# Performance work log

Measured on AMD Instinct MI355X. Metric: run time of the kernel, lower is better.

The kernel has to match this reference:

```python
import jax, jax.numpy as jnp
import numpy as np

N = 100000
E = 1600000
D = 128

NEG_SLOPE = 0.1


def _leaky(x):
    return jnp.where(x >= 0, x, NEG_SLOPE * x)


def _ising_gcn(x, row, col, val, n, W=None, b=None, bias=None):
    # scatter_mean of |val| over source rows -> custom diagonal
    abs_val = jnp.abs(val)
    cnt = jax.ops.segment_sum(jnp.ones_like(abs_val), row, num_segments=n)
    abs_mean = jax.ops.segment_sum(abs_val, row, num_segments=n) / jnp.maximum(cnt, 1.0)
    diag = jnp.arange(n, dtype=row.dtype)
    frow = jnp.concatenate([row, diag])
    fcol = jnp.concatenate([col, diag])
    fval = jnp.concatenate([val, abs_mean])
    # symmetric normalization on |values|: v / sqrt(deg[row] * deg[col])
    deg = jax.ops.segment_sum(jnp.abs(fval), frow, num_segments=n)
    dinv = jnp.where(deg > 0, jax.lax.rsqrt(deg), 0.0)
    pv = fval * dinv[frow] * dinv[fcol]
    if W is not None:
        x = x @ W.T + b
    # propagate: out[col] += pv * x[row]  (PyG source_to_target, aggr='add')
    out = jax.ops.segment_sum(pv[:, None] * x[frow], fcol, num_segments=n)
    if bias is not None:
        out = out + bias
    return out


def setup_inputs() -> dict:
    key = jax.random.key(0)
    ks = jax.random.split(key, 10)
    edge_index = jax.random.randint(ks[0], (2, E), 0, N, dtype=jnp.int64)
    edge_val = jax.random.normal(ks[1], (E,), dtype=jnp.float32)
    s1 = 1.0 / np.sqrt(1.0)
    s2 = 1.0 / np.sqrt(D)
    s3 = 1.0 / np.sqrt(2 * D)
    return {
        "edge_index": edge_index,
        "edge_val": edge_val,
        "n_nodes": N,
        "w1": jax.random.uniform(ks[2], (D, 1), jnp.float32, -s1, s1),
        "b1": jax.random.uniform(ks[3], (D,), jnp.float32, -s1, s1),
        "w2": jax.random.uniform(ks[4], (2 * D, D), jnp.float32, -s2, s2),
        "b2": jax.random.uniform(ks[5], (2 * D,), jnp.float32, -s2, s2),
        "bias2": jnp.zeros((2 * D,), jnp.float32),
        "w3": jax.random.uniform(ks[6], (D, 2 * D), jnp.float32, -s3, s3),
        "b3": jax.random.uniform(ks[7], (D,), jnp.float32, -s3, s3),
        "bias3": jnp.zeros((D,), jnp.float32),
    }


def reference(edge_index, edge_val, n_nodes, w1, b1, w2, b2, bias2, w3, b3, bias3):
    row, col = edge_index[0], edge_index[1]
    x = jnp.ones((n_nodes, 1), dtype=edge_val.dtype)
    # conv1: no W, no bias (1 -> 1)
    x = _ising_gcn(x, row, col, edge_val, n_nodes)
    # linear 1 -> D, leaky relu (dropout omitted: inference)
    x = _leaky(x @ w1.T + b1)
    # conv2: D -> 2D with lin + bias
    x = _leaky(_ising_gcn(x, row, col, edge_val, n_nodes, W=w2, b=b2, bias=bias2))
    # conv3: 2D -> D with lin + bias
    x = _leaky(_ising_gcn(x, row, col, edge_val, n_nodes, W=w3, b=b3, bias=bias3))
    return x
```

## Files before the change

### kernel.cpp

```cpp
#include <hip/hip_runtime.h>
#include <hip/hip_bf16.h>

#define NEG_SLOPE 0.1f
#define D1 128
#define D2 256

#define BSH 7
#define NPB 128
#define EPB 2048
#define MAXBUK 1024

__device__ __forceinline__ float leaky(float x) { return x >= 0.f ? x : NEG_SLOPE * x; }

__device__ __forceinline__ unsigned short f2bf(float x) {
    union { float f; unsigned int u; } v; v.f = x;
    unsigned int r = (v.u + 0x7FFFu + ((v.u >> 16) & 1u)) >> 16;
    return (unsigned short)r;
}

__device__ __forceinline__ unsigned int pk2bf(float a, float b) {
    return (unsigned int)f2bf(a) | ((unsigned int)f2bf(b) << 16);
}

__device__ __forceinline__ int ts_g(const int* __restrict__ TS,
                                    const int* __restrict__ partials, int idx) {
    return TS[idx] + partials[idx >> 11];
}

__global__ __launch_bounds__(256) void k_hist(const int* __restrict__ row,
                                              const int* __restrict__ col,
                                              int* __restrict__ T,
                                              int E, int NBLK, int NBUK)
{
    __shared__ int hc[MAXBUK], hr[MAXBUK];
    for (int b = threadIdx.x; b < NBUK; b += 256) { hc[b] = 0; hr[b] = 0; }
    __syncthreads();
    int base = blockIdx.x * EPB;
#pragma unroll
    for (int i = 0; i < 8; i++) {
        int e = base + i * 256 + threadIdx.x;
        if (e < E) {
            atomicAdd(&hc[col[e] >> BSH], 1);
            atomicAdd(&hr[row[e] >> BSH], 1);
        }
    }
    __syncthreads();
    int NT = NBUK * NBLK;
    for (int b = threadIdx.x; b < NBUK; b += 256) {
        T[b * NBLK + blockIdx.x]      = hc[b];
        T[NT + b * NBLK + blockIdx.x] = hr[b];
    }
}

__global__ __launch_bounds__(256) void k_scan_local(const int* __restrict__ in, int* __restrict__ out,
                                                    int* __restrict__ partials, int n)
{
    __shared__ int s[256];
    int base = blockIdx.x * 2048 + threadIdx.x * 8;
    int v[8]; int sum = 0;
#pragma unroll
    for (int i = 0; i < 8; i++) { v[i] = (base + i < n) ? in[base + i] : 0; sum += v[i]; }
    s[threadIdx.x] = sum;
    __syncthreads();
    for (int off = 1; off < 256; off <<= 1) {
        int t = (threadIdx.x >= off) ? s[threadIdx.x - off] : 0;
        __syncthreads();
        s[threadIdx.x] += t;
        __syncthreads();
    }
    int excl = s[threadIdx.x] - sum;
#pragma unroll
    for (int i = 0; i < 8; i++) { if (base + i < n) { out[base + i] = excl; excl += v[i]; } }
    if (threadIdx.x == 255) partials[blockIdx.x] = s[255];
}

__global__ __launch_bounds__(1024) void k_scan_partials_par(int* __restrict__ partials, int nb)
{
    __shared__ int s[1024];
    int t = threadIdx.x;
    int v = (t < nb) ? partials[t] : 0;
    s[t] = v;
    __syncthreads();
    for (int off = 1; off < 1024; off <<= 1) {
        int u = (t >= off) ? s[t - off] : 0;
        __syncthreads();
        s[t] += u;
        __syncthreads();
    }
    if (t < nb) partials[t] = s[t] - v;
}

__global__ __launch_bounds__(256) void k_scat(const int* __restrict__ row,
                                              const int* __restrict__ col,
                                              const float* __restrict__ val,
                                              const int* __restrict__ TS,
                                              const int* __restrict__ partials,
                                              int2* __restrict__ X, int2* __restrict__ Y,
                                              int E, int NBLK, int NBUK)
{
    __shared__ int oc[MAXBUK], orw[MAXBUK];
    int NT = NBUK * NBLK;
    for (int b = threadIdx.x; b < NBUK; b += 256) {
        oc[b]  = ts_g(TS, partials, b * NBLK + blockIdx.x);
        orw[b] = ts_g(TS, partials, NT + b * NBLK + blockIdx.x);
    }
    __syncthreads();
    int base = blockIdx.x * EPB;
#pragma unroll
    for (int i = 0; i < 8; i++) {
        int e = base + i * 256 + threadIdx.x;
        if (e < E) {
            int r = row[e], c = col[e];
            float v = val[e];
            int pc = atomicAdd(&oc[c >> BSH], 1);
            X[pc] = make_int2(((c & (NPB - 1)) << 25) | r, __float_as_int(v));
            int pr = atomicAdd(&orw[r >> BSH], 1);
            Y[pr - E] = make_int2(r & (NPB - 1), __float_as_int(fabsf(v)));
        }
    }
}

__global__ __launch_bounds__(256) void k_rowstats(const int2* __restrict__ Y,
                                                  const int* __restrict__ TS,
                                                  const int* __restrict__ partials,
                                                  float* __restrict__ dinv,
                                                  float* __restrict__ pv_self,
                                                  int N, int E, int NBLK, int NBUK)
{
    __shared__ float fs[NPB];
    __shared__ int   cn[NPB];
    int t = threadIdx.x;
    if (t < NPB) { fs[t] = 0.f; cn[t] = 0; }
    __syncthreads();
    int NT = NBUK * NBLK;
    int buk = blockIdx.x;
    int s = ts_g(TS, partials, NT + buk * NBLK);
    int e = (buk == NBUK - 1) ? 2 * E : ts_g(TS, partials, NT + (buk + 1) * NBLK);
    for (int j = s + t; j < e; j += 256) {
        int2 y = Y[j - E];
        atomicAdd(&fs[y.x], __int_as_float(y.y));
        atomicAdd(&cn[y.x], 1);
    }
    __syncthreads();
    if (t < NPB) {
        int node = buk * NPB + t;
        if (node < N) {
            float as = fs[t];
            float c  = (float)cn[t];
            float am = as / fmaxf(c, 1.f);
            float deg = as + am;
            float di = deg > 0.f ? rsqrtf(deg) : 0.f;
            dinv[node]    = di;
            pv_self[node] = am * di * di;
        }
    }
}

__global__ __launch_bounds__(256) void k_colfinal(const int2* __restrict__ X,
                                                  const int* __restrict__ TS,
                                                  const int* __restrict__ partials,
                                                  const float* __restrict__ dinv,
                                                  const float* __restrict__ pv_self,
                                                  int* __restrict__ col_ptr,
                                                  int2* __restrict__ srt_rp,
                                                  float* __restrict__ x1,
                                                  int N, int E, int NBLK, int NBUK)
{
    __shared__ int   hist[NPB];
    __shared__ int   tmp[NPB];
    __shared__ int   rb[NPB];
    __shared__ float xs[NPB];
    __shared__ float dl[NPB];
    int t = threadIdx.x;
    int buk = blockIdx.x;
    int node = buk * NPB + t;
    if (t < NPB) {
        hist[t] = 0; xs[t] = 0.f;
        dl[t] = (node < N) ? dinv[node] : 0.f;
    }
    __syncthreads();
    int s  = ts_g(TS, partials, buk * NBLK);
    int e2 = (buk == NBUK - 1) ? E : ts_g(TS, partials, (buk + 1) * NBLK);
    for (int j = s + t; j < e2; j += 256) {
        unsigned xw = (unsigned)X[j].x;
        atomicAdd(&hist[xw >> 25], 1);
    }
    __syncthreads();
    if (t < NPB) tmp[t] = hist[t];
    __syncthreads();
    for (int off = 1; off < NPB; off <<= 1) {
        int u = (t >= off && t < NPB) ? tmp[t - off] : 0;
        __syncthreads();
        if (t < NPB) tmp[t] += u;
        __syncthreads();
    }
    if (t < NPB) {
        int excl = tmp[t] - hist[t];
        rb[t] = s + excl;
        if (node < N) col_ptr[node] = s + excl;
    }
    if (buk == NBUK - 1 && t == 0) col_ptr[N] = E;
    __syncthreads();
    for (int j = s + t; j < e2; j += 256) {
        int2 xx = X[j];
        unsigned xw = (unsigned)xx.x;
        int cl = xw >> 25;
        int r  = (int)(xw & 0x1FFFFFFu);
        float p = __int_as_float(xx.y) * dinv[r] * dl[cl];
        int pos = atomicAdd(&rb[cl], 1);
        srt_rp[pos] = make_int2(r, __float_as_int(p));
        atomicAdd(&xs[cl], p);
    }
    __syncthreads();
    if (t < NPB && node < N) x1[node] = pv_self[node] + xs[t];
}

__global__ __launch_bounds__(256) void k_prop2b(const int* __restrict__ col_ptr,
                                                const int2* __restrict__ srt_rp,
                                                const float* __restrict__ pv_self,
                                                const float* __restrict__ x1,
                                                const float* __restrict__ w1,
                                                const float* __restrict__ b1,
                                                unsigned int* __restrict__ p2b, int N)
{
    int node = blockIdx.x * 4 + (threadIdx.x >> 6);
    int lane = threadIdx.x & 63;
    if (node >= N) return;

    float2 w = *(const float2*)&w1[lane * 2];
    float2 b = *(const float2*)&b1[lane * 2];
    float ps  = pv_self[node];
    float x1n = x1[node];
    float acc0 = ps * leaky(fmaf(x1n, w.x, b.x));
    float acc1 = ps * leaky(fmaf(x1n, w.y, b.y));

    int s = col_ptr[node], e = col_ptr[node + 1];
    for (int base = s; base < e; base += 64) {
        int mc = min(64, e - base);
        float p = 0.f, sv = 0.f;
        if (lane < mc) {
            int2 rp = srt_rp[base + lane];
            p  = __int_as_float(rp.y);
            sv = x1[rp.x];
        }
        for (int k = 0; k < mc; ++k) {
            float pk = __shfl(p, k, 64);
            float sk = __shfl(sv, k, 64);
            acc0 += pk * leaky(fmaf(sk, w.x, b.x));
            acc1 += pk * leaky(fmaf(sk, w.y, b.y));
        }
    }

    p2b[(size_t)node * 64 + lane] = pk2bf(acc0, acc1);
}

__global__ __launch_bounds__(256) void k_prop3_bf16(const int* __restrict__ col_ptr,
                                                    const int2* __restrict__ srt_rp,
                                                    const float* __restrict__ pv_self,
                                                    const unsigned int* __restrict__ zb,
                                                    const float* __restrict__ bias3,
                                                    float* __restrict__ out, int N)
{
    int node = blockIdx.x * 4 + (threadIdx.x >> 6);
    int lane = threadIdx.x & 63;
    if (node >= N) return;

    unsigned int us = zb[(size_t)node * 64 + lane];
    float ps = pv_self[node];
    float acc0 = ps * __uint_as_float(us << 16);
    float acc1 = ps * __uint_as_float(us & 0xFFFF0000u);

    int j = col_ptr[node], e = col_ptr[node + 1];
    for (; j + 3 < e; j += 4) {
        int2 rp0 = srt_rp[j];
        int2 rp1 = srt_rp[j + 1];
        int2 rp2 = srt_rp[j + 2];
        int2 rp3 = srt_rp[j + 3];
        unsigned int u0 = zb[(size_t)rp0.x * 64 + lane];
        unsigned int u1 = zb[(size_t)rp1.x * 64 + lane];
        unsigned int u2 = zb[(size_t)rp2.x * 64 + lane];
        unsigned int u3 = zb[(size_t)rp3.x * 64 + lane];
        float p0 = __int_as_float(rp0.y);
        float p1 = __int_as_float(rp1.y);
        float p2 = __int_as_float(rp2.y);
        float p3 = __int_as_float(rp3.y);
        acc0 += p0 * __uint_as_float(u0 << 16);
        acc1 += p0 * __uint_as_float(u0 & 0xFFFF0000u);
        acc0 += p1 * __uint_as_float(u1 << 16);
        acc1 += p1 * __uint_as_float(u1 & 0xFFFF0000u);
        acc0 += p2 * __uint_as_float(u2 << 16);
        acc1 += p2 * __uint_as_float(u2 & 0xFFFF0000u);
        acc0 += p3 * __uint_as_float(u3 << 16);
        acc1 += p3 * __uint_as_float(u3 & 0xFFFF0000u);
    }
    for (; j < e; ++j) {
        int2 rp = srt_rp[j];
        unsigned int u = zb[(size_t)rp.x * 64 + lane];
        float p = __int_as_float(rp.y);
        acc0 += p * __uint_as_float(u << 16);
        acc1 += p * __uint_as_float(u & 0xFFFF0000u);
    }

    float2 b = *(const float2*)&bias3[lane * 2];
    float2 o = make_float2(leaky(acc0 + b.x), leaky(acc1 + b.y));
    *(float2*)&out[(size_t)node * D1 + lane * 2] = o;
}

__global__ __launch_bounds__(256) void k_gemm_fused(const unsigned int* __restrict__ p2b,
                                                    const float* __restrict__ w2,
                                                    const float* __restrict__ b2,
                                                    const float* __restrict__ bias2,
                                                    const float* __restrict__ w3,
                                                    const float* __restrict__ b3,
                                                    const float* __restrict__ x1,
                                                    unsigned short* __restrict__ zb,
                                                    int N)
{
    typedef __attribute__((ext_vector_type(8))) short short8v;
    typedef __attribute__((ext_vector_type(4))) float f32x4;

    __shared__ unsigned short Al[64 * 40];
    __shared__ unsigned short Bl[256 * 40];
    __shared__ unsigned short H[64 * 264];

    const int t = threadIdx.x;
    const int n_base = blockIdx.x * 64;
    const int l  = t & 63, wid = t >> 6;
    const int lr = l & 15,  lk = l >> 4;

    f32x4 acc1[4][4] = {};
    {
        const int arow = t >> 2, ach = t & 3;
        const bool aok = (n_base + arow) < N;
        for (int k0 = 0; k0 < D1; k0 += 32) {
            uint4 ua = make_uint4(0u, 0u, 0u, 0u);
            if (aok) ua = *(const uint4*)&p2b[(size_t)(n_base + arow) * 64 + (k0 >> 1) + ach * 4];
            const float* pw = w2 + (size_t)t * D1 + k0;
            float4 c0 = *(const float4*)(pw);
            float4 c1 = *(const float4*)(pw + 4);
            float4 c2 = *(const float4*)(pw + 8);
            float4 c3 = *(const float4*)(pw + 12);
            float4 c4 = *(const float4*)(pw + 16);
            float4 c5 = *(const float4*)(pw + 20);
            float4 c6 = *(const float4*)(pw + 24);
            float4 c7 = *(const float4*)(pw + 28);
            __syncthreads();
            *(uint4*)&Al[arow * 40 + ach * 8] = ua;
            uint4 u0 = make_uint4(pk2bf(c0.x, c0.y), pk2bf(c0.z, c0.w),
                                  pk2bf(c1.x, c1.y), pk2bf(c1.z, c1.w));
            uint4 u1 = make_uint4(pk2bf(c2.x, c2.y), pk2bf(c2.z, c2.w),
                                  pk2bf(c3.x, c3.y), pk2bf(c3.z, c3.w));
            uint4 u2 = make_uint4(pk2bf(c4.x, c4.y), pk2bf(c4.z, c4.w),
                                  pk2bf(c5.x, c5.y), pk2bf(c5.z, c5.w));
            uint4 u3 = make_uint4(pk2bf(c6.x, c6.y), pk2bf(c6.z, c6.w),
                                  pk2bf(c7.x, c7.y), pk2bf(c7.z, c7.w));
            *(uint4*)&Bl[t * 40 + 0]  = u0;
            *(uint4*)&Bl[t * 40 + 8]  = u1;
            *(uint4*)&Bl[t * 40 + 16] = u2;
            *(uint4*)&Bl[t * 40 + 24] = u3;
            __syncthreads();

            short8v af[4], bf[4];
#pragma unroll
            for (int i = 0; i < 4; i++) {
                af[i] = *(const short8v*)&Al[(i * 16 + lr) * 40 + lk * 8];
                bf[i] = *(const short8v*)&Bl[(wid * 64 + i * 16 + lr) * 40 + lk * 8];
            }
#pragma unroll
            for (int i = 0; i < 4; i++)
#pragma unroll
                for (int j = 0; j < 4; j++)
                    acc1[i][j] = __builtin_amdgcn_mfma_f32_16x16x32_bf16(af[i], bf[j], acc1[i][j], 0, 0, 0);
        }
    }

    {
        float xv[4][4];
#pragma unroll
        for (int i = 0; i < 4; i++)
#pragma unroll
            for (int q = 0; q < 4; q++) {
                int node = n_base + i * 16 + lk * 4 + q;
                xv[i][q] = (node < N) ? x1[node] : 0.f;
            }
#pragma unroll
        for (int j = 0; j < 4; j++) {
            const int col = wid * 64 + j * 16 + lr;
            const float bv = b2[col];
            const float bi = bias2[col];
#pragma unroll
            for (int i = 0; i < 4; i++)
#pragma unroll
                for (int q = 0; q < 4; q++) {
                    int rloc = i * 16 + lk * 4 + q;
                    float v = acc1[i][j][q] + xv[i][q] * bv + bi;
                    H[rloc * 264 + col] = ((n_base + rloc) < N) ? f2bf(leaky(v)) : (unsigned short)0;
                }
        }
    }
    __syncthreads();

    f32x4 acc2[4][2] = {};
    {
        const int m = t >> 1, hf = t & 1;
        for (int k0 = 0; k0 < D2; k0 += 32) {
            const float* pw = w3 + (size_t)m * D2 + k0 + hf * 16;
            float4 c0 = *(const float4*)(pw);
            float4 c1 = *(const float4*)(pw + 4);
            float4 c2 = *(const float4*)(pw + 8);
            float4 c3 = *(const float4*)(pw + 12);
            __syncthreads();
            uint4 u0 = make_uint4(pk2bf(c0.x, c0.y), pk2bf(c0.z, c0.w),
                                  pk2bf(c1.x, c1.y), pk2bf(c1.z, c1.w));
            uint4 u1 = make_uint4(pk2bf(c2.x, c2.y), pk2bf(c2.z, c2.w),
                                  pk2bf(c3.x, c3.y), pk2bf(c3.z, c3.w));
            *(uint4*)&Bl[m * 40 + hf * 16 + 0] = u0;
            *(uint4*)&Bl[m * 40 + hf * 16 + 8] = u1;
            __syncthreads();

            short8v af[4], bf[2];
#pragma unroll
            for (int i = 0; i < 4; i++)
                af[i] = *(const short8v*)&H[(i * 16 + lr) * 264 + k0 + lk * 8];
#pragma unroll
            for (int j = 0; j < 2; j++)
                bf[j] = *(const short8v*)&Bl[(wid * 32 + j * 16 + lr) * 40 + lk * 8];
#pragma unroll
            for (int i = 0; i < 4; i++)
#pragma unroll
                for (int j = 0; j < 2; j++)
                    acc2[i][j] = __builtin_amdgcn_mfma_f32_16x16x32_bf16(af[i], bf[j], acc2[i][j], 0, 0, 0);
        }
    }

#pragma unroll
    for (int j = 0; j < 2; j++) {
        const int col = wid * 32 + j * 16 + lr;
        const float bv = b3[col];
#pragma unroll
        for (int i = 0; i < 4; i++)
#pragma unroll
            for (int q = 0; q < 4; q++) {
                int node = n_base + i * 16 + lk * 4 + q;
                if (node < N)
                    zb[(size_t)node * D1 + col] = f2bf(acc2[i][j][q] + bv);
            }
    }
}

extern "C" void kernel_launch(void* const* d_in, const int* in_sizes, int n_in,
                              void* d_out, int out_size, void* d_ws, size_t ws_size,
                              hipStream_t stream)
{
    const int* ei       = (const int*)d_in[0];
    const float* val    = (const float*)d_in[1];
    const float* w1     = (const float*)d_in[3];
    const float* b1     = (const float*)d_in[4];
    const float* w2     = (const float*)d_in[5];
    const float* b2     = (const float*)d_in[6];
    const float* bias2  = (const float*)d_in[7];
    const float* w3     = (const float*)d_in[8];
    const float* b3     = (const float*)d_in[9];
    const float* bias3  = (const float*)d_in[10];
    float* out = (float*)d_out;

    const int E = in_sizes[1];
    const int N = out_size / D1;
    const int* row = ei;
    const int* col = ei + E;

    const int NBLK = (E + EPB - 1) / EPB;
    const int NBUK = (N + NPB - 1) >> BSH;
    const int NT   = NBUK * NBLK;

    float* dinv    = (float*)d_ws;
    float* pv_self = dinv + N;
    float* x1      = pv_self + N;
    int*   col_ptr = (int*)(x1 + N);
    int*   partials= col_ptr + N + 8;
    int2*  srt_rp  = (int2*)(partials + 1024);
    unsigned int* p2b = (unsigned int*)(srt_rp + (size_t)E);
    int*   TS      = (int*)(p2b + (size_t)N * 64);
    int*   T       = TS + (size_t)2 * NT;
    int2*  Y       = (int2*)(T + (size_t)2 * NT);
    int2* X = (int2*)p2b;
    unsigned short* zb = (unsigned short*)p2b;

    const int B = 256;
    const int n2 = 2 * NT;
    const int scan_blocks = (n2 + 2047) / 2048;

    k_hist<<<NBLK, B, 0, stream>>>(row, col, T, E, NBLK, NBUK);
    k_scan_local<<<scan_blocks, 256, 0, stream>>>(T, TS, partials, n2);
    k_scan_partials_par<<<1, 1024, 0, stream>>>(partials, scan_blocks);
    k_scat<<<NBLK, B, 0, stream>>>(row, col, val, TS, partials, X, Y, E, NBLK, NBUK);
    k_rowstats<<<NBUK, B, 0, stream>>>(Y, TS, partials, dinv, pv_self, N, E, NBLK, NBUK);
    k_colfinal<<<NBUK, B, 0, stream>>>(X, TS, partials, dinv, pv_self, col_ptr, srt_rp, x1, N, E, NBLK, NBUK);

    k_prop2b<<<(N + 3) / 4, 256, 0, stream>>>(col_ptr, srt_rp, pv_self, x1, w1, b1, p2b, N);
    k_gemm_fused<<<(N + 63) / 64, 256, 0, stream>>>(p2b, w2, b2, bias2, w3, b3, x1, zb, N);

    k_prop3_bf16<<<(N + 3) / 4, 256, 0, stream>>>(col_ptr, srt_rp, pv_self, (const unsigned int*)zb, bias3, out, N);
}
```

Measured before the change: 413.7 us.

## Pre-convert weights to MFMA-ready bf16 layout and drop per-block weight staging

```diff
diff --git a/kernel.cpp b/kernel.cpp
--- a/kernel.cpp
+++ b/kernel.cpp
@@ -306,145 +306,132 @@
     *(float2*)&out[(size_t)node * D1 + lane * 2] = o;
 }
 
-__global__ __launch_bounds__(256) void k_gemm_fused(const unsigned int* __restrict__ p2b,
-                                                    const float* __restrict__ w2,
-                                                    const float* __restrict__ b2,
-                                                    const float* __restrict__ bias2,
-                                                    const float* __restrict__ w3,
-                                                    const float* __restrict__ b3,
-                                                    const float* __restrict__ x1,
-                                                    unsigned short* __restrict__ zb,
-                                                    int N)
+__global__ __launch_bounds__(256) void k_cvtw(const float* __restrict__ w2,
+                                              const float* __restrict__ w3,
+                                              unsigned short* __restrict__ w2f,
+                                              unsigned short* __restrict__ w3f)
+{
+    int i = blockIdx.x * 256 + threadIdx.x;
+    {
+        int m = i >> 7, k = i & 127;
+        w2f[(((k >> 3) * 256 + m) << 3) + (k & 7)] = f2bf(w2[i]);
+    }
+    {
+        int m = i >> 8, k = i & 255;
+        w3f[(((k >> 3) * 128 + m) << 3) + (k & 7)] = f2bf(w3[i]);
+    }
+}
+
+__global__ __launch_bounds__(256, 3) void k_gemm_fused2(const unsigned int* __restrict__ p2b,
+                                                        const unsigned short* __restrict__ w2f,
+                                                        const float* __restrict__ b2,
+                                                        const float* __restrict__ bias2,
+                                                        const unsigned short* __restrict__ w3f,
+                                                        const float* __restrict__ b3,
+                                                        const float* __restrict__ x1,
+                                                        unsigned short* __restrict__ zb,
+                                                        int N)
 {
     typedef __attribute__((ext_vector_type(8))) short short8v;
     typedef __attribute__((ext_vector_type(4))) float f32x4;
 
-    __shared__ unsigned short Al[64 * 40];
-    __shared__ unsigned short Bl[256 * 40];
-    __shared__ unsigned short H[64 * 264];
+    __shared__ unsigned short Ak[16 * 64 * 8];
+    __shared__ unsigned short H [32 * 64 * 8];
 
     const int t = threadIdx.x;
     const int n_base = blockIdx.x * 64;
     const int l  = t & 63, wid = t >> 6;
-    const int lr = l & 15,  lk = l >> 4;
+    const int lr = l & 15, lk = l >> 4;
+
+    {
+        const int node = t & 63, kb0 = t >> 6;
+        const bool ok = (n_base + node) < N;
+        const unsigned int* src = p2b + (size_t)(n_base + node) * 64;
+#pragma unroll
+        for (int kk = 0; kk < 4; kk++) {
+            int kblk = kk * 4 + kb0;
+            uint4 v = ok ? *(const uint4*)(src + kblk * 4) : make_uint4(0u, 0u, 0u, 0u);
+            *(uint4*)&Ak[(kblk * 64 + node) * 8] = v;
+        }
+    }
+    __syncthreads();
 
     f32x4 acc1[4][4] = {};
+#pragma unroll
+    for (int k0 = 0; k0 < D1; k0 += 32) {
+        short8v af[4], bf[4];
+#pragma unroll
+        for (int i = 0; i < 4; i++)
+            af[i] = *(const short8v*)&w2f[((((k0 >> 3) + lk) * 256) + wid * 64 + i * 16 + lr) * 8];
+#pragma unroll
+        for (int j = 0; j < 4; j++)
+            bf[j] = *(const short8v*)&Ak[(((k0 >> 3) + lk) * 64 + j * 16 + lr) * 8];
+#pragma unroll
+        for (int i = 0; i < 4; i++)
+#pragma unroll
+            for (int j = 0; j < 4; j++)
+                acc1[i][j] = __builtin_amdgcn_mfma_f32_16x16x32_bf16(af[i], bf[j], acc1[i][j], 0, 0, 0);
+    }
+
     {
-        const int arow = t >> 2, ach = t & 3;
-        const bool aok = (n_base + arow) < N;
-        for (int k0 = 0; k0 < D1; k0 += 32) {
-            uint4 ua = make_uint4(0u, 0u, 0u, 0u);
-            if (aok) ua = *(const uint4*)&p2b[(size_t)(n_base + arow) * 64 + (k0 >> 1) + ach * 4];
-            const float* pw = w2 + (size_t)t * D1 + k0;
-            float4 c0 = *(const float4*)(pw);
-            float4 c1 = *(const float4*)(pw + 4);
-            float4 c2 = *(const float4*)(pw + 8);
-            float4 c3 = *(const float4*)(pw + 12);
-            float4 c4 = *(const float4*)(pw + 16);
-            float4 c5 = *(const float4*)(pw + 20);
-            float4 c6 = *(const float4*)(pw + 24);
-            float4 c7 = *(const float4*)(pw + 28);
-            __syncthreads();
-            *(uint4*)&Al[arow * 40 + ach * 8] = ua;
-            uint4 u0 = make_uint4(pk2bf(c0.x, c0.y), pk2bf(c0.z, c0.w),
-                                  pk2bf(c1.x, c1.y), pk2bf(c1.z, c1.w));
-            uint4 u1 = make_uint4(pk2bf(c2.x, c2.y), pk2bf(c2.z, c2.w),
-                                  pk2bf(c3.x, c3.y), pk2bf(c3.z, c3.w));
-            uint4 u2 = make_uint4(pk2bf(c4.x, c4.y), pk2bf(c4.z, c4.w),
-                                  pk2bf(c5.x, c5.y), pk2bf(c5.z, c5.w));
-            uint4 u3 = make_uint4(pk2bf(c6.x, c6.y), pk2bf(c6.z, c6.w),
-                                  pk2bf(c7.x, c7.y), pk2bf(c7.z, c7.w));
-            *(uint4*)&Bl[t * 40 + 0]  = u0;
-            *(uint4*)&Bl[t * 40 + 8]  = u1;
-            *(uint4*)&Bl[t * 40 + 16] = u2;
-            *(uint4*)&Bl[t * 40 + 24] = u3;
-            __syncthreads();
-
-            short8v af[4], bf[4];
-#pragma unroll
-            for (int i = 0; i < 4; i++) {
-                af[i] = *(const short8v*)&Al[(i * 16 + lr) * 40 + lk * 8];
-                bf[i] = *(const short8v*)&Bl[(wid * 64 + i * 16 + lr) * 40 + lk * 8];
+        float xv[4];
+#pragma unroll
+        for (int j = 0; j < 4; j++) {
+            int node = n_base + j * 16 + lr;
+            xv[j] = (node < N) ? x1[node] : 0.f;
+        }
+#pragma unroll
+        for (int i = 0; i < 4; i++) {
+            const int c0 = wid * 64 + i * 16 + lk * 4;
+            float4 bq  = *(const float4*)&b2[c0];
+            float4 biq = *(const float4*)&bias2[c0];
+            const int kblk = wid * 8 + i * 2 + (lk >> 1);
+#pragma unroll
+            for (int j = 0; j < 4; j++) {
+                float v0 = leaky(acc1[i][j][0] + xv[j] * bq.x + biq.x);
+                float v1 = leaky(acc1[i][j][1] + xv[j] * bq.y + biq.y);
+                float v2 = leaky(acc1[i][j][2] + xv[j] * bq.z + biq.z);
+                float v3 = leaky(acc1[i][j][3] + xv[j] * bq.w + biq.w);
+                uint2 pk = make_uint2(pk2bf(v0, v1), pk2bf(v2, v3));
+                *(uint2*)&H[(kblk * 64 + j * 16 + lr) * 8 + (lk & 1) * 4] = pk;
             }
-#pragma unroll
-            for (int i = 0; i < 4; i++)
-#pragma unroll
-                for (int j = 0; j < 4; j++)
-                    acc1[i][j] = __builtin_amdgcn_mfma_f32_16x16x32_bf16(af[i], bf[j], acc1[i][j], 0, 0, 0);
-        }
-    }
-
-    {
-        float xv[4][4];
-#pragma unroll
-        for (int i = 0; i < 4; i++)
-#pragma unroll
-            for (int q = 0; q < 4; q++) {
-                int node = n_base + i * 16 + lk * 4 + q;
-                xv[i][q] = (node < N) ? x1[node] : 0.f;
+        }
+    }
+    __syncthreads();
+
+    f32x4 acc2[2][4] = {};
+#pragma unroll
+    for (int k0 = 0; k0 < D2; k0 += 32) {
+        short8v af[2], bf[4];
+#pragma unroll
+        for (int i = 0; i < 2; i++)
+            af[i] = *(const short8v*)&w3f[((((k0 >> 3) + lk) * 128) + wid * 32 + i * 16 + lr) * 8];
+#pragma unroll
+        for (int j = 0; j < 4; j++)
+            bf[j] = *(const short8v*)&H[(((k0 >> 3) + lk) * 64 + j * 16 + lr) * 8];
+#pragma unroll
+        for (int i = 0; i < 2; i++)
+#pragma unroll
+            for (int j = 0; j < 4; j++)
+                acc2[i][j] = __builtin_amdgcn_mfma_f32_16x16x32_bf16(af[i], bf[j], acc2[i][j], 0, 0, 0);
+    }
+
+#pragma unroll
+    for (int i = 0; i < 2; i++) {
+        const int m0 = wid * 32 + i * 16 + lk * 4;
+        float4 bq = *(const float4*)&b3[m0];
+#pragma unroll
+        for (int j = 0; j < 4; j++) {
+            int node = n_base + j * 16 + lr;
+            if (node < N) {
+                ushort4 s4;
+                s4.x = f2bf(acc2[i][j][0] + bq.x);
+                s4.y = f2bf(acc2[i][j][1] + bq.y);
+                s4.z = f2bf(acc2[i][j][2] + bq.z);
+                s4.w = f2bf(acc2[i][j][3] + bq.w);
+                *(ushort4*)&zb[(size_t)node * D1 + m0] = s4;
             }
-#pragma unroll
-        for (int j = 0; j < 4; j++) {
-            const int col = wid * 64 + j * 16 + lr;
-            const float bv = b2[col];
-            const float bi = bias2[col];
-#pragma unroll
-            for (int i = 0; i < 4; i++)
-#pragma unroll
-                for (int q = 0; q < 4; q++) {
-                    int rloc = i * 16 + lk * 4 + q;
-                    float v = acc1[i][j][q] + xv[i][q] * bv + bi;
-                    H[rloc * 264 + col] = ((n_base + rloc) < N) ? f2bf(leaky(v)) : (unsigned short)0;
-                }
-        }
-    }
-    __syncthreads();
-
-    f32x4 acc2[4][2] = {};
-    {
-        const int m = t >> 1, hf = t & 1;
-        for (int k0 = 0; k0 < D2; k0 += 32) {
-            const float* pw = w3 + (size_t)m * D2 + k0 + hf * 16;
-            float4 c0 = *(const float4*)(pw);
-            float4 c1 = *(const float4*)(pw + 4);
-            float4 c2 = *(const float4*)(pw + 8);
-            float4 c3 = *(const float4*)(pw + 12);
-            __syncthreads();
-            uint4 u0 = make_uint4(pk2bf(c0.x, c0.y), pk2bf(c0.z, c0.w),
-                                  pk2bf(c1.x, c1.y), pk2bf(c1.z, c1.w));
-            uint4 u1 = make_uint4(pk2bf(c2.x, c2.y), pk2bf(c2.z, c2.w),
-                                  pk2bf(c3.x, c3.y), pk2bf(c3.z, c3.w));
-            *(uint4*)&Bl[m * 40 + hf * 16 + 0] = u0;
-            *(uint4*)&Bl[m * 40 + hf * 16 + 8] = u1;
-            __syncthreads();
-
-            short8v af[4], bf[2];
-#pragma unroll
-            for (int i = 0; i < 4; i++)
-                af[i] = *(const short8v*)&H[(i * 16 + lr) * 264 + k0 + lk * 8];
-#pragma unroll
-            for (int j = 0; j < 2; j++)
-                bf[j] = *(const short8v*)&Bl[(wid * 32 + j * 16 + lr) * 40 + lk * 8];
-#pragma unroll
-            for (int i = 0; i < 4; i++)
-#pragma unroll
-                for (int j = 0; j < 2; j++)
-                    acc2[i][j] = __builtin_amdgcn_mfma_f32_16x16x32_bf16(af[i], bf[j], acc2[i][j], 0, 0, 0);
-        }
-    }
-
-#pragma unroll
-    for (int j = 0; j < 2; j++) {
-        const int col = wid * 32 + j * 16 + lr;
-        const float bv = b3[col];
-#pragma unroll
-        for (int i = 0; i < 4; i++)
-#pragma unroll
-            for (int q = 0; q < 4; q++) {
-                int node = n_base + i * 16 + lk * 4 + q;
-                if (node < N)
-                    zb[(size_t)node * D1 + col] = f2bf(acc2[i][j][q] + bv);
-            }
+        }
     }
 }
 
@@ -483,6 +470,8 @@
     int*   TS      = (int*)(p2b + (size_t)N * 64);
     int*   T       = TS + (size_t)2 * NT;
     int2*  Y       = (int2*)(T + (size_t)2 * NT);
+    unsigned short* w2f = (unsigned short*)(Y + (size_t)E);
+    unsigned short* w3f = w2f + 32768;
     int2* X = (int2*)p2b;
     unsigned short* zb = (unsigned short*)p2b;
 
@@ -497,8 +486,10 @@
     k_rowstats<<<NBUK, B, 0, stream>>>(Y, TS, partials, dinv, pv_self, N, E, NBLK, NBUK);
     k_colfinal<<<NBUK, B, 0, stream>>>(X, TS, partials, dinv, pv_self, col_ptr, srt_rp, x1, N, E, NBLK, NBUK);
 
+    k_cvtw<<<128, 256, 0, stream>>>(w2, w3, w2f, w3f);
+
     k_prop2b<<<(N + 3) / 4, 256, 0, stream>>>(col_ptr, srt_rp, pv_self, x1, w1, b1, p2b, N);
-    k_gemm_fused<<<(N + 63) / 64, 256, 0, stream>>>(p2b, w2, b2, bias2, w3, b3, x1, zb, N);
+    k_gemm_fused2<<<(N + 63) / 64, 256, 0, stream>>>(p2b, w2f, b2, bias2, w3f, b3, x1, zb, N);
 
     k_prop3_bf16<<<(N + 3) / 4, 256, 0, stream>>>(col_ptr, srt_rp, pv_self, (const unsigned int*)zb, bias3, out, N);
 }
```

New measurement: 368.7 us. -10.9%, faster.
